# Kernel optimization log

Measured on AMD Instinct MI355X. Metric: run time of the kernel, lower is better.

The kernel has to match this reference:

```python
import jax, jax.numpy as jnp
import numpy as np

LOG2 = float(np.log(2.0))
INV_SQRT3 = float(1.0 / np.sqrt(3.0))

def ssp(x):
    # ShiftedSoftPlus: softplus(x) - log(2)
    return jax.nn.softplus(x) - LOG2

def setup_inputs() -> dict:
    key = jax.random.key(0)
    ks = jax.random.split(key, 13)
    N, E, M, A, R, H = 50000, 800000, 32, 16, 8, 64
    return {
        "node_feats": jax.random.normal(ks[0], (N, 4 * M), dtype=jnp.float32),  # 32x0e + 32x1o flat
        "node_attrs": jax.random.normal(ks[1], (N, A), dtype=jnp.float32),
        "edge_embedding": jax.random.uniform(ks[2], (E, R), dtype=jnp.float32),  # radial basis, 0e
        "edge_attrs": jax.random.normal(ks[3], (E, 4), dtype=jnp.float32),  # SH: 1x0e + 1x1o
        "edge_index": jax.random.randint(ks[4], (2, E), 0, N),
        "W1s": jax.random.normal(ks[5], (M, M), dtype=jnp.float32),
        "W1v": jax.random.normal(ks[6], (M, M), dtype=jnp.float32),
        "Wr0": jax.random.normal(ks[7], (R, H), dtype=jnp.float32),
        "Wr1": jax.random.normal(ks[8], (H, 4 * M), dtype=jnp.float32),  # tp.weight_numel = 4 paths * 32 mul
        "W2s": jax.random.normal(ks[9], (2 * M, M), dtype=jnp.float32),
        "W2v": jax.random.normal(ks[10], (2 * M, M), dtype=jnp.float32),
        "Wsc_s": jax.random.normal(ks[11], (M, A, M), dtype=jnp.float32),
        "Wsc_v": jax.random.normal(ks[12], (M, A, M), dtype=jnp.float32),
    }

def reference(node_feats, node_attrs, edge_embedding, edge_attrs, edge_index,
              W1s, W1v, Wr0, Wr1, W2s, W2v, Wsc_s, Wsc_v):
    N = node_feats.shape[0]
    M = 32           # multiplicity of each irrep
    A = node_attrs.shape[1]
    AVG_NEIGH = 16.0
    # split flat irreps features: [N,32] scalars (0e), [N,32,3] vectors (1o)
    s_in = node_feats[:, :M]
    v_in = node_feats[:, M:].reshape(N, M, 3)

    # linear_1: per-irrep channel mixing, e3nn 1/sqrt(fan_in) normalization
    inv_m = 1.0 / float(np.sqrt(M))
    s = (s_in @ W1s) * inv_m                                  # [N,32]
    v = jnp.einsum('nmc,mk->nkc', v_in, W1v) * inv_m          # [N,32,3]

    # radial MLP on edge scalars -> per-edge tensor-product path weights [E,4,32]
    h = ssp((edge_embedding @ Wr0) * (1.0 / float(np.sqrt(edge_embedding.shape[1]))))
    w = (h @ Wr1) * (1.0 / float(np.sqrt(h.shape[1])))
    w = w.reshape(-1, 4, M)
    w0, w1, w2, w3 = w[:, 0], w[:, 1], w[:, 2], w[:, 3]

    src, dst = edge_index[0], edge_index[1]
    ss = s[src]                                               # [E,32]
    vv = v[src]                                               # [E,32,3]
    e0 = edge_attrs[:, :1]                                    # [E,1]  Y_0
    e1 = edge_attrs[:, 1:4]                                   # [E,3]  Y_1

    # weighted CG tensor product, 'uvu' paths (component normalization)
    m0 = w0 * ss * e0                                                   # 0e x 0e -> 0e
    m3 = w3 * jnp.einsum('emc,ec->em', vv, e1) * INV_SQRT3              # 1o x 1o -> 0e
    m1 = w1[:, :, None] * ss[:, :, None] * e1[:, None, :]               # 0e x 1o -> 1o
    m2 = w2[:, :, None] * vv * e0[:, :, None]                           # 1o x 0e -> 1o
    mid_s = jnp.concatenate([m0, m3], axis=1)                           # [E,64]
    mid_v = jnp.concatenate([m1, m2], axis=1)                           # [E,64,3]

    # scatter-sum to destination nodes
    ns = jax.ops.segment_sum(mid_s, dst, num_segments=N)
    nv = jax.ops.segment_sum(mid_v, dst, num_segments=N)
    neigh = 1.0 / float(np.sqrt(AVG_NEIGH))

    # linear_2 on simplified mid irreps 64x0e + 64x1o
    inv2 = 1.0 / float(np.sqrt(2 * M))
    out_s = (ns @ W2s) * (inv2 * neigh)
    out_v = jnp.einsum('nmc,mk->nkc', nv, W2v) * (inv2 * neigh)

    # self connection: FullyConnectedTensorProduct(node_feats_in, node_attrs)
    fc = 1.0 / float(np.sqrt(M * A))
    out_s = out_s + jnp.einsum('nu,na,uaw->nw', s_in, node_attrs, Wsc_s) * fc
    out_v = out_v + jnp.einsum('nuc,na,uaw->nwc', v_in, node_attrs, Wsc_v) * fc

    return jnp.concatenate([out_s, out_v.reshape(N, 3 * M)], axis=1)
```

## Files before the change

### kernel.cpp

```cpp
#include <hip/hip_runtime.h>
#include <stdint.h>
#include <math.h>

typedef __attribute__((ext_vector_type(8))) short bf16x8;
typedef __attribute__((ext_vector_type(4))) float f32x4;

__device__ __forceinline__ unsigned short f2bf(float f){
  unsigned int u = __float_as_uint(f);
  u += 0x7fffu + ((u >> 16) & 1u);
  return (unsigned short)(u >> 16);
}

__device__ __forceinline__ float bf2f(short s){
  return __uint_as_float(((unsigned int)(unsigned short)s) << 16);
}

__device__ __forceinline__ float ssp_f(float x){
  float u = exp2f(-fabsf(x)*1.4426950408889634f);
  return fmaxf(x, 0.f) + 0.6931471805599453f*(__log2f(1.0f + u) - 1.0f);
}

__global__ void k_count_prep(const int* __restrict__ eidx, int E, int* __restrict__ cnt,
                             const float* __restrict__ Wr0, const float* __restrict__ Wr1,
                             const float* __restrict__ Wsc_s, const float* __restrict__ Wsc_v,
                             const float* __restrict__ W1s, const float* __restrict__ W1v,
                             unsigned short* __restrict__ wr1frag, float* __restrict__ wr0p,
                             unsigned short* __restrict__ wscfrag, unsigned short* __restrict__ w1frag){
  int id = blockIdx.x*256 + threadIdx.x;
  if(id < 512) wr0p[id] = Wr0[(id & 7)*64 + (id >> 3)];
  if(id < 1024){
    int fi = id >> 6, lane = id & 63;
    int c0 = lane & 15, g = lane >> 4;
    int kt = fi >> 3, ct = fi & 7;
    unsigned short tmp[8];
    #pragma unroll
    for(int i = 0; i < 8; i++){
      int k = kt*32 + g*8 + i;
      tmp[i] = f2bf(Wr1[k*128 + ct*16 + c0]);
    }
    #pragma unroll
    for(int i = 0; i < 8; i++) wr1frag[id*8 + i] = tmp[i];
  }
  if(id < 4096){
    int sel  = id >> 11;
    int fi   = (id >> 6) & 31;
    int lane = id & 63;
    int c0 = lane & 15, g = lane >> 4;
    int ks = fi >> 1, ct = fi & 1;
    const float* W = sel ? Wsc_v : Wsc_s;
    bf16x8 tmp;
    #pragma unroll
    for(int i = 0; i < 8; i++){
      int k = ks*32 + g*8 + i;
      tmp[i] = (short)f2bf(W[k*32 + ct*16 + c0]);
    }
    *(bf16x8*)&wscfrag[(size_t)id*8] = tmp;
  }
  if(id < 256){
    int sel = id >> 7, ct = (id >> 6) & 1, lane = id & 63;
    int c0 = lane & 15, g = lane >> 4;
    const float* W = sel ? W1v : W1s;
    bf16x8 tmp;
    #pragma unroll
    for(int i = 0; i < 8; i++){
      int m = g*8 + i;
      tmp[i] = (short)f2bf(W[m*32 + ct*16 + c0]);
    }
    *(bf16x8*)&w1frag[(size_t)id*8] = tmp;
  }
  if(id < E) atomicAdd(&cnt[eidx[E + id]], 1);
}

__global__ void k_scan_a(const int* __restrict__ cnt, int N, int* __restrict__ offs, int* __restrict__ bsum){
  __shared__ int arr[1024];
  int t = threadIdx.x, i = blockIdx.x*1024 + t;
  int v = (i < N) ? cnt[i] : 0;
  int own = v;
  arr[t] = v;
  for(int off = 1; off < 1024; off <<= 1){
    __syncthreads();
    int u = (t >= off) ? arr[t - off] : 0;
    __syncthreads();
    arr[t] += u;
  }
  if(i < N) offs[i] = arr[t] - own;
  if(t == 1023) bsum[blockIdx.x] = arr[1023];
}

__global__ void k_scan_b(int* __restrict__ bsum, int NB, int* __restrict__ offs, int N){
  if(threadIdx.x == 0 && blockIdx.x == 0){
    int run = 0;
    for(int b = 0; b < NB; b++){ int t = bsum[b]; bsum[b] = run; run += t; }
    offs[N] = run;
  }
}

__global__ void k_scan_c(int* __restrict__ offs, const int* __restrict__ bsum, int* __restrict__ cursor, int N){
  int i = blockIdx.x*1024 + threadIdx.x;
  if(i < N){
    int v = offs[i] + bsum[blockIdx.x];
    offs[i] = v;
    cursor[i] = v;
  }
}

__global__ void k_perm(const float* __restrict__ eemb, const float* __restrict__ eattr,
                       const int* __restrict__ eidx, int E, int* __restrict__ cursor,
                       int* __restrict__ src_perm, float* __restrict__ eattr_perm,
                       float* __restrict__ eemb_perm){
  int e = blockIdx.x*256 + threadIdx.x;
  if(e < E){
    int d = eidx[E + e];
    int dp = atomicAdd(&cursor[d], 1);
    src_perm[dp] = eidx[e];
    *(f32x4*)(eattr_perm + (size_t)dp*4) = *(const f32x4*)(eattr + (size_t)e*4);
    *(f32x4*)(eemb_perm + (size_t)dp*8)     = *(const f32x4*)(eemb + (size_t)e*8);
    *(f32x4*)(eemb_perm + (size_t)dp*8 + 4) = *(const f32x4*)(eemb + (size_t)e*8 + 4);
  }
}

__global__ __launch_bounds__(256) void k_node(
    const float* __restrict__ nf, const float* __restrict__ na,
    const unsigned short* __restrict__ w1frag,
    const unsigned short* __restrict__ wscfrag,
    unsigned short* __restrict__ sv, float* __restrict__ out, int N)
{
  __shared__ float xl[64*133];
  __shared__ __align__(16) float al[64*20];
  const int t = threadIdx.x;
  const int n0 = blockIdx.x*64;

  for(int idx = t; idx < 64*128; idx += 256){
    int r = idx >> 7, c = idx & 127;
    int n = n0 + r;
    xl[r*133 + c] = (n < N) ? nf[(size_t)n*128 + c] : 0.f;
  }
  for(int idx = t; idx < 64*16; idx += 256){
    int r = idx >> 4, c = idx & 15;
    int n = n0 + r;
    al[r*20 + c] = (n < N) ? na[(size_t)n*16 + c] : 0.f;
  }
  __syncthreads();

  const float INVM = 0.17677669529663689f;
  const float FC   = 0.044194173824159216f;

  const int lane = t & 63, wv = t >> 6;
  const int c0 = lane & 15, g = lane >> 4;

  {
    const unsigned short* w1f = w1frag + (size_t)((wv == 0) ? 0 : 1024);
    bf16x8 b0 = *(const bf16x8*)&w1f[(0*64 + lane)*8];
    bf16x8 b1 = *(const bf16x8*)&w1f[(1*64 + lane)*8];
    #pragma unroll
    for(int rt = 0; rt < 4; rt++){
      int row = rt*16 + c0;
      bf16x8 a;
      #pragma unroll
      for(int i = 0; i < 8; i++){
        int m = g*8 + i;
        float xv = (wv == 0) ? xl[row*133 + m] : xl[row*133 + 32 + 3*m + (wv-1)];
        a[i] = (short)f2bf(xv);
      }
      f32x4 z = {0.f,0.f,0.f,0.f};
      f32x4 d0 = __builtin_amdgcn_mfma_f32_16x16x32_bf16(a, b0, z, 0, 0, 0);
      f32x4 d1 = __builtin_amdgcn_mfma_f32_16x16x32_bf16(a, b1, z, 0, 0, 0);
      #pragma unroll
      for(int r = 0; r < 4; r++){
        int node = n0 + rt*16 + g*4 + r;
        if(node < N){
          sv[(size_t)node*128 + c0*8 + wv*2 + 0] = f2bf(d0[r]*INVM);
          sv[(size_t)node*128 + c0*8 + wv*2 + 1] = f2bf(d1[r]*INVM);
        }
      }
    }
  }

  const unsigned short* wf = wscfrag + (size_t)((wv == 0) ? 0 : 16384);

  f32x4 accm[4][2];
  #pragma unroll
  for(int rt = 0; rt < 4; rt++)
    #pragma unroll
    for(int ct = 0; ct < 2; ct++) accm[rt][ct] = (f32x4){0.f,0.f,0.f,0.f};

  for(int ks = 0; ks < 16; ks++){
    bf16x8 bfr[2];
    bfr[0] = *(const bf16x8*)&wf[(size_t)((ks*2 + 0)*64 + lane)*8];
    bfr[1] = *(const bf16x8*)&wf[(size_t)((ks*2 + 1)*64 + lane)*8];
    int u2 = ks*2 + (g >> 1);
    int ab = (g & 1)*8;
    #pragma unroll
    for(int rt = 0; rt < 4; rt++){
      int row = rt*16 + c0;
      float xv = (wv == 0) ? xl[row*133 + u2] : xl[row*133 + 32 + 3*u2 + (wv-1)];
      f32x4 v0 = *(const f32x4*)&al[row*20 + ab];
      f32x4 v1 = *(const f32x4*)&al[row*20 + ab + 4];
      bf16x8 a;
      a[0] = (short)f2bf(xv*v0[0]); a[1] = (short)f2bf(xv*v0[1]);
      a[2] = (short)f2bf(xv*v0[2]); a[3] = (short)f2bf(xv*v0[3]);
      a[4] = (short)f2bf(xv*v1[0]); a[5] = (short)f2bf(xv*v1[1]);
      a[6] = (short)f2bf(xv*v1[2]); a[7] = (short)f2bf(xv*v1[3]);
      #pragma unroll
      for(int ct = 0; ct < 2; ct++)
        accm[rt][ct] = __builtin_amdgcn_mfma_f32_16x16x32_bf16(a, bfr[ct], accm[rt][ct], 0, 0, 0);
    }
  }

  #pragma unroll
  for(int rt = 0; rt < 4; rt++)
    #pragma unroll
    for(int ct = 0; ct < 2; ct++)
      #pragma unroll
      for(int i = 0; i < 4; i++){
        int node = n0 + rt*16 + g*4 + i;
        if(node < N){
          int col = ct*16 + c0;
          float v = accm[rt][ct][i] * FC;
          if(wv == 0) out[(size_t)node*128 + col] = v;
          else        out[(size_t)node*128 + 32 + 3*col + (wv-1)] = v;
        }
      }
}

__global__ __launch_bounds__(256, 4) void k_wedge(
    const float* __restrict__ eemb_perm,
    const unsigned short* __restrict__ wr1frag, const float* __restrict__ wr0p,
    unsigned short* __restrict__ wper, int NB16, int E)
{
  __shared__ __align__(16) float wr0t[512];
  __shared__ __align__(16) unsigned short bwl[8192];
  const int t = threadIdx.x;
  {
    const f32x4* s4 = (const f32x4*)wr1frag;
    f32x4* d4 = (f32x4*)bwl;
    #pragma unroll
    for(int i = 0; i < 4; i++) d4[t + i*256] = s4[t + i*256];
    if(t < 128) ((f32x4*)wr0t)[t] = ((const f32x4*)wr0p)[t];
  }
  __syncthreads();

  const int lane = t & 63;
  const int wv   = t >> 6;
  const int c0   = lane & 15;
  const int g    = lane >> 4;
  const float S8 = 0.35355339059327373f;

  int p = blockIdx.x*4 + wv;
  if(p >= NB16) return;
  int p16 = p*16;
  int bc = E - p16; if(bc > 16) bc = 16;
  bool val = (c0 < bc);

  size_t row = (size_t)(p16 + (val ? c0 : 0))*8;
  f32x4 p0 = *(const f32x4*)(eemb_perm + row);
  f32x4 p1 = *(const f32x4*)(eemb_perm + row + 4);
  float ee[8];
  ee[0]=p0[0]; ee[1]=p0[1]; ee[2]=p0[2]; ee[3]=p0[3];
  ee[4]=p1[0]; ee[5]=p1[1]; ee[6]=p1[2]; ee[7]=p1[3];

  bf16x8 afr[2];
  #pragma unroll
  for(int kt = 0; kt < 2; kt++){
    bf16x8 a;
    #pragma unroll
    for(int i = 0; i < 8; i++){
      int j = kt*32 + g*8 + i;
      f32x4 wa = *(const f32x4*)&wr0t[j*8];
      f32x4 wb = *(const f32x4*)&wr0t[j*8 + 4];
      float pre = ee[0]*wa[0] + ee[1]*wa[1] + ee[2]*wa[2] + ee[3]*wa[3]
                + ee[4]*wb[0] + ee[5]*wb[1] + ee[6]*wb[2] + ee[7]*wb[3];
      a[i] = (short)f2bf(ssp_f(pre * S8));
    }
    afr[kt] = a;
  }

  f32x4 cfr[8];
  #pragma unroll
  for(int ct = 0; ct < 8; ct++) cfr[ct] = (f32x4){0.f,0.f,0.f,0.f};
  #pragma unroll
  for(int kt = 0; kt < 2; kt++)
    #pragma unroll
    for(int ct = 0; ct < 8; ct++){
      bf16x8 bfr = *(const bf16x8*)&bwl[((kt*8 + ct)*64 + lane)*8];
      cfr[ct] = __builtin_amdgcn_mfma_f32_16x16x32_bf16(afr[kt], bfr, cfr[ct], 0, 0, 0);
    }

  #pragma unroll
  for(int i = 0; i < 4; i++){
    if(g*4 + i < bc){
      bf16x8 wpk;
      #pragma unroll
      for(int ct = 0; ct < 8; ct++) wpk[ct] = (short)f2bf(cfr[ct][i] * 0.125f);
      *(bf16x8*)(wper + (size_t)(p16 + g*4 + i)*128 + c0*8) = wpk;
    }
  }
}

__global__ __launch_bounds__(256, 4) void k_msg(
    const unsigned short* __restrict__ sv, const unsigned short* __restrict__ wper,
    const float* __restrict__ eattr_perm, const int* __restrict__ src_perm,
    const int* __restrict__ offs, const float* __restrict__ W2s,
    const float* __restrict__ W2v, float* __restrict__ out, int N)
{
  __shared__ __align__(16) float nsl[4][256];
  __shared__ __align__(16) float w2sT[32*68];
  __shared__ __align__(16) float w2vT[32*68];
  const int t = threadIdx.x, lane = t & 63, wv = t >> 6;
  const int c0 = lane & 15, g = lane >> 4;

  {
    #pragma unroll
    for(int i = 0; i < 8; i++){
      int idx = t + i*256;
      int m = idx >> 5, o = idx & 31;
      w2sT[o*68 + m] = W2s[idx];
      w2vT[o*68 + m] = W2v[idx];
    }
  }
  __syncthreads();

  const int n = blockIdx.x*4 + wv;
  if(n >= N) return;

  const float SC2 = 0.03125f;
  const float IS3 = 0.57735026918962576f;

  float acc[16];
  #pragma unroll
  for(int i = 0; i < 16; i++) acc[i] = 0.f;

  const int eb0 = offs[n], eb1 = offs[n+1];
  for(int eb = eb0; eb < eb1; eb += 16){
    int bc = eb1 - eb; if(bc > 16) bc = 16;
    #pragma unroll
    for(int r = 0; r < 4; r++){
      int es = r*4 + g;
      if(es >= bc) continue;
      int e = eb + es;
      int s = src_perm[e];
      bf16x8 sr = *(const bf16x8*)(sv + (size_t)s*128 + c0*8);
      f32x4 ea = *(const f32x4*)(eattr_perm + (size_t)e*4);
      bf16x8 w8 = *(const bf16x8*)(wper + (size_t)e*128 + c0*8);
      float w0A = bf2f(w8[0]), w0B = bf2f(w8[1]);
      float w1A = bf2f(w8[2]), w1B = bf2f(w8[3]);
      float w2A = bf2f(w8[4]), w2B = bf2f(w8[5]);
      float w3A = bf2f(w8[6]), w3B = bf2f(w8[7]);
      float ssA = bf2f(sr[0]), ssB = bf2f(sr[1]);
      float vA0 = bf2f(sr[2]), vB0 = bf2f(sr[3]);
      float vA1 = bf2f(sr[4]), vB1 = bf2f(sr[5]);
      float vA2 = bf2f(sr[6]), vB2 = bf2f(sr[7]);
      float e0 = ea[0], e1x = ea[1], e1y = ea[2], e1z = ea[3];

      acc[0] += w0A*ssA*e0;
      acc[1] += w0B*ssB*e0;
      acc[2] += w3A*(vA0*e1x + vA1*e1y + vA2*e1z);
      acc[3] += w3B*(vB0*e1x + vB1*e1y + vB2*e1z);
      float h1A = w1A*ssA, h1B = w1B*ssB;
      acc[4]  += h1A*e1x; acc[5]  += h1A*e1y; acc[6]  += h1A*e1z;
      acc[7]  += h1B*e1x; acc[8]  += h1B*e1y; acc[9]  += h1B*e1z;
      float h2A = w2A*e0, h2B = w2B*e0;
      acc[10] += h2A*vA0; acc[11] += h2A*vA1; acc[12] += h2A*vA2;
      acc[13] += h2B*vB0; acc[14] += h2B*vB1; acc[15] += h2B*vB2;
    }
  }

  #pragma unroll
  for(int i = 0; i < 16; i++){
    acc[i] += __shfl_xor(acc[i], 16);
    acc[i] += __shfl_xor(acc[i], 32);
  }

  float* nl = nsl[wv];
  if(g == 0){
    nl[c0]      = acc[0];
    nl[16 + c0] = acc[1];
    nl[32 + c0] = acc[2]*IS3;
    nl[48 + c0] = acc[3]*IS3;
    #pragma unroll
    for(int cc = 0; cc < 3; cc++){
      nl[64 + cc*64 +  0 + c0] = acc[4  + cc];
      nl[64 + cc*64 + 16 + c0] = acc[7  + cc];
      nl[64 + cc*64 + 32 + c0] = acc[10 + cc];
      nl[64 + cc*64 + 48 + c0] = acc[13 + cc];
    }
  }
  __threadfence_block();

  const int t1 = lane, t2 = 64 + lane;
  int u1 = t1 - 32; if(u1 < 0) u1 = 0;
  const int w1i = u1/3, c1i = u1%3;
  const int w2i = (t2 - 32)/3, c2i = (t2 - 32)%3;
  const f32x4* p1a = (const f32x4*)((t1 < 32) ? &nl[0] : &nl[64 + c1i*64]);
  const f32x4* p1b = (const f32x4*)((t1 < 32) ? &w2sT[t1*68] : &w2vT[w1i*68]);
  const f32x4* p2a = (const f32x4*)&nl[64 + c2i*64];
  const f32x4* p2b = (const f32x4*)&w2vT[w2i*68];
  float s1 = 0.f, s2 = 0.f;
  #pragma unroll
  for(int q = 0; q < 16; q++){
    f32x4 a = p1a[q], b = p1b[q];
    f32x4 c = p2a[q], d = p2b[q];
    s1 += a[0]*b[0] + a[1]*b[1] + a[2]*b[2] + a[3]*b[3];
    s2 += c[0]*d[0] + c[1]*d[1] + c[2]*d[2] + c[3]*d[3];
  }
  out[(size_t)n*128 + t1] += s1*SC2;
  out[(size_t)n*128 + t2] += s2*SC2;
}

extern "C" void kernel_launch(void* const* d_in, const int* in_sizes, int n_in,
                              void* d_out, int out_size, void* d_ws, size_t ws_size,
                              hipStream_t stream)
{
  const float* nf    = (const float*)d_in[0];
  const float* na    = (const float*)d_in[1];
  const float* eemb  = (const float*)d_in[2];
  const float* eattr = (const float*)d_in[3];
  const int*   eidx  = (const int*)d_in[4];
  const float* W1s   = (const float*)d_in[5];
  const float* W1v   = (const float*)d_in[6];
  const float* Wr0   = (const float*)d_in[7];
  const float* Wr1   = (const float*)d_in[8];
  const float* W2s   = (const float*)d_in[9];
  const float* W2v   = (const float*)d_in[10];
  const float* Wsc_s = (const float*)d_in[11];
  const float* Wsc_v = (const float*)d_in[12];
  float* out = (float*)d_out;

  int N = in_sizes[0]/128;
  int E = in_sizes[2]/8;
  int NB16 = (E + 15)/16;

  char* ws = (char*)d_ws;
  size_t off = 0;
  unsigned short* sv = (unsigned short*)(ws + off); off += (size_t)N*128*2;
  unsigned short* wper = (unsigned short*)(ws + off); off += (size_t)NB16*16*128*2;
  float* eemb_perm = (float*)(ws + off);      off += (size_t)NB16*16*8*4;
  float* eattr_perm = (float*)(ws + off);     off += (size_t)NB16*16*4*4;
  int* src_perm = (int*)(ws + off);           off += (size_t)NB16*16*4;
  int* cnt    = (int*)(ws + off);             off += (size_t)N*4;
  int* offs   = (int*)(ws + off);             off += (size_t)(N+1)*4;
  int* cursor = (int*)(ws + off);             off += (size_t)N*4;
  int* bsum   = (int*)(ws + off);             off += 4096;
  unsigned short* wr1frag = (unsigned short*)(ws + off); off += 16384;
  float* wr0p = (float*)(ws + off);           off += 2048;
  unsigned short* wscfrag = (unsigned short*)(ws + off); off += 65536;
  unsigned short* w1frag = (unsigned short*)(ws + off);  off += 4096;

  int NB = (N + 1023)/1024;

  (void)hipMemsetAsync(cnt, 0, (size_t)N*4, stream);
  k_count_prep<<<dim3((E+255)/256), dim3(256), 0, stream>>>(eidx, E, cnt, Wr0, Wr1,
                                                            Wsc_s, Wsc_v, W1s, W1v,
                                                            wr1frag, wr0p, wscfrag, w1frag);
  k_scan_a <<<dim3(NB),          dim3(1024),0, stream>>>(cnt, N, offs, bsum);
  k_scan_b <<<dim3(1),           dim3(64),  0, stream>>>(bsum, NB, offs, N);
  k_scan_c <<<dim3(NB),          dim3(1024),0, stream>>>(offs, bsum, cursor, N);
  k_perm   <<<dim3((E+255)/256), dim3(256), 0, stream>>>(eemb, eattr, eidx, E, cursor,
                                                         src_perm, eattr_perm, eemb_perm);
  k_node   <<<dim3((N+63)/64),   dim3(256), 0, stream>>>(nf, na, w1frag, wscfrag, sv, out, N);
  k_wedge  <<<dim3((NB16+3)/4),  dim3(256), 0, stream>>>(eemb_perm, wr1frag, wr0p, wper, NB16, E);
  k_msg    <<<dim3((N+3)/4),     dim3(256), 0, stream>>>(sv, wper, eattr_perm, src_perm, offs,
                                                         W2s, W2v, out, N);
}
```

Before: 337.9 us.

## Split linear_2 out of message kernel into separate bf16 MFMA kernel

The per-node W2 projection moves out of k_msg, which used scalar FP32 dot products and loaded the transposed W2 into LDS in every block. k_msg now stores the aggregated 256-wide node message as bf16 to a buffer that reuses the eemb_perm workspace. A new k_out kernel applies W2s/W2v with bf16 MFMA over 64-node tiles, using weight fragments pre-packed in the prep kernel. This lightens k_msg (no LDS weight staging, fewer registers) at the cost of an extra launch, a bf16 round trip of node messages through global memory, and reduced precision in the projection.

```diff
diff --git a/kernel.cpp b/kernel.cpp
--- a/kernel.cpp
+++ b/kernel.cpp
@@ -3,6 +3,7 @@
 #include <math.h>
 
 typedef __attribute__((ext_vector_type(8))) short bf16x8;
+typedef __attribute__((ext_vector_type(4))) short s16x4;
 typedef __attribute__((ext_vector_type(4))) float f32x4;
 
 __device__ __forceinline__ unsigned short f2bf(float f){
@@ -24,8 +25,10 @@
                              const float* __restrict__ Wr0, const float* __restrict__ Wr1,
                              const float* __restrict__ Wsc_s, const float* __restrict__ Wsc_v,
                              const float* __restrict__ W1s, const float* __restrict__ W1v,
+                             const float* __restrict__ W2s, const float* __restrict__ W2v,
                              unsigned short* __restrict__ wr1frag, float* __restrict__ wr0p,
-                             unsigned short* __restrict__ wscfrag, unsigned short* __restrict__ w1frag){
+                             unsigned short* __restrict__ wscfrag, unsigned short* __restrict__ w1frag,
+                             unsigned short* __restrict__ w2frag){
   int id = blockIdx.x*256 + threadIdx.x;
   if(id < 512) wr0p[id] = Wr0[(id & 7)*64 + (id >> 3)];
   if(id < 1024){
@@ -67,6 +70,19 @@
       tmp[i] = (short)f2bf(W[m*32 + ct*16 + c0]);
     }
     *(bf16x8*)&w1frag[(size_t)id*8] = tmp;
+  }
+  if(id < 512){
+    int fi = id >> 6, lane = id & 63;
+    int c0 = lane & 15, g = lane >> 4;
+    int sel = fi >> 2, kt = (fi >> 1) & 1, ct = fi & 1;
+    const float* W = sel ? W2v : W2s;
+    bf16x8 tmp;
+    #pragma unroll
+    for(int i = 0; i < 8; i++){
+      int k = kt*32 + g*8 + i;
+      tmp[i] = (short)f2bf(W[k*32 + ct*16 + c0]);
+    }
+    *(bf16x8*)&w2frag[(size_t)id*8] = tmp;
   }
   if(id < E) atomicAdd(&cnt[eidx[E + id]], 1);
 }
@@ -300,30 +316,15 @@
 __global__ __launch_bounds__(256, 4) void k_msg(
     const unsigned short* __restrict__ sv, const unsigned short* __restrict__ wper,
     const float* __restrict__ eattr_perm, const int* __restrict__ src_perm,
-    const int* __restrict__ offs, const float* __restrict__ W2s,
-    const float* __restrict__ W2v, float* __restrict__ out, int N)
+    const int* __restrict__ offs, unsigned short* __restrict__ nsv, int N)
 {
   __shared__ __align__(16) float nsl[4][256];
-  __shared__ __align__(16) float w2sT[32*68];
-  __shared__ __align__(16) float w2vT[32*68];
   const int t = threadIdx.x, lane = t & 63, wv = t >> 6;
   const int c0 = lane & 15, g = lane >> 4;
 
-  {
-    #pragma unroll
-    for(int i = 0; i < 8; i++){
-      int idx = t + i*256;
-      int m = idx >> 5, o = idx & 31;
-      w2sT[o*68 + m] = W2s[idx];
-      w2vT[o*68 + m] = W2v[idx];
-    }
-  }
-  __syncthreads();
-
   const int n = blockIdx.x*4 + wv;
   if(n >= N) return;
 
-  const float SC2 = 0.03125f;
   const float IS3 = 0.57735026918962576f;
 
   float acc[16];
@@ -387,24 +388,56 @@
   }
   __threadfence_block();
 
-  const int t1 = lane, t2 = 64 + lane;
-  int u1 = t1 - 32; if(u1 < 0) u1 = 0;
-  const int w1i = u1/3, c1i = u1%3;
-  const int w2i = (t2 - 32)/3, c2i = (t2 - 32)%3;
-  const f32x4* p1a = (const f32x4*)((t1 < 32) ? &nl[0] : &nl[64 + c1i*64]);
-  const f32x4* p1b = (const f32x4*)((t1 < 32) ? &w2sT[t1*68] : &w2vT[w1i*68]);
-  const f32x4* p2a = (const f32x4*)&nl[64 + c2i*64];
-  const f32x4* p2b = (const f32x4*)&w2vT[w2i*68];
-  float s1 = 0.f, s2 = 0.f;
-  #pragma unroll
-  for(int q = 0; q < 16; q++){
-    f32x4 a = p1a[q], b = p1b[q];
-    f32x4 c = p2a[q], d = p2b[q];
-    s1 += a[0]*b[0] + a[1]*b[1] + a[2]*b[2] + a[3]*b[3];
-    s2 += c[0]*d[0] + c[1]*d[1] + c[2]*d[2] + c[3]*d[3];
-  }
-  out[(size_t)n*128 + t1] += s1*SC2;
-  out[(size_t)n*128 + t2] += s2*SC2;
+  f32x4 v4 = *(const f32x4*)&nl[lane*4];
+  s16x4 o4;
+  o4[0] = (short)f2bf(v4[0]); o4[1] = (short)f2bf(v4[1]);
+  o4[2] = (short)f2bf(v4[2]); o4[3] = (short)f2bf(v4[3]);
+  *(s16x4*)(nsv + (size_t)n*256 + lane*4) = o4;
+}
+
+__global__ __launch_bounds__(256) void k_out(
+    const unsigned short* __restrict__ nsv, const unsigned short* __restrict__ w2frag,
+    float* __restrict__ out, int N)
+{
+  const int t = threadIdx.x, lane = t & 63, wv = t >> 6;
+  const int c0 = lane & 15, g = lane >> 4;
+  const int n0 = blockIdx.x*64;
+  const float SC2 = 0.03125f;
+  const int sel = (wv == 0) ? 0 : 1;
+
+  bf16x8 bfr[2][2];
+  #pragma unroll
+  for(int kt = 0; kt < 2; kt++)
+    #pragma unroll
+    for(int ct = 0; ct < 2; ct++)
+      bfr[kt][ct] = *(const bf16x8*)&w2frag[(size_t)(((sel*2 + kt)*2 + ct)*64 + lane)*8];
+
+  #pragma unroll
+  for(int rt = 0; rt < 4; rt++){
+    int na_ = n0 + rt*16 + c0; if(na_ >= N) na_ = N - 1;
+    const unsigned short* ap = nsv + (size_t)na_*256 + wv*64;
+    bf16x8 a0 = *(const bf16x8*)(ap + g*8);
+    bf16x8 a1 = *(const bf16x8*)(ap + 32 + g*8);
+    f32x4 accq[2];
+    #pragma unroll
+    for(int ct = 0; ct < 2; ct++){
+      f32x4 z = {0.f,0.f,0.f,0.f};
+      f32x4 d = __builtin_amdgcn_mfma_f32_16x16x32_bf16(a0, bfr[0][ct], z, 0, 0, 0);
+      d = __builtin_amdgcn_mfma_f32_16x16x32_bf16(a1, bfr[1][ct], d, 0, 0, 0);
+      accq[ct] = d;
+    }
+    #pragma unroll
+    for(int ct = 0; ct < 2; ct++)
+      #pragma unroll
+      for(int i = 0; i < 4; i++){
+        int node = n0 + rt*16 + g*4 + i;
+        if(node < N){
+          int col = ct*16 + c0;
+          size_t idx = (size_t)node*128 + ((wv == 0) ? col : 32 + 3*col + (wv-1));
+          out[idx] += accq[ct][i]*SC2;
+        }
+      }
+  }
 }
 
 extern "C" void kernel_launch(void* const* d_in, const int* in_sizes, int n_in,
@@ -435,6 +468,7 @@
   unsigned short* sv = (unsigned short*)(ws + off); off += (size_t)N*128*2;
   unsigned short* wper = (unsigned short*)(ws + off); off += (size_t)NB16*16*128*2;
   float* eemb_perm = (float*)(ws + off);      off += (size_t)NB16*16*8*4;
+  unsigned short* nsv = (unsigned short*)eemb_perm;
   float* eattr_perm = (float*)(ws + off);     off += (size_t)NB16*16*4*4;
   int* src_perm = (int*)(ws + off);           off += (size_t)NB16*16*4;
   int* cnt    = (int*)(ws + off);             off += (size_t)N*4;
@@ -445,13 +479,14 @@
   float* wr0p = (float*)(ws + off);           off += 2048;
   unsigned short* wscfrag = (unsigned short*)(ws + off); off += 65536;
   unsigned short* w1frag = (unsigned short*)(ws + off);  off += 4096;
+  unsigned short* w2frag = (unsigned short*)(ws + off);  off += 8192;
 
   int NB = (N + 1023)/1024;
 
   (void)hipMemsetAsync(cnt, 0, (size_t)N*4, stream);
   k_count_prep<<<dim3((E+255)/256), dim3(256), 0, stream>>>(eidx, E, cnt, Wr0, Wr1,
-                                                            Wsc_s, Wsc_v, W1s, W1v,
-                                                            wr1frag, wr0p, wscfrag, w1frag);
+                                                            Wsc_s, Wsc_v, W1s, W1v, W2s, W2v,
+                                                            wr1frag, wr0p, wscfrag, w1frag, w2frag);
   k_scan_a <<<dim3(NB),          dim3(1024),0, stream>>>(cnt, N, offs, bsum);
   k_scan_b <<<dim3(1),           dim3(64),  0, stream>>>(bsum, NB, offs, N);
   k_scan_c <<<dim3(NB),          dim3(1024),0, stream>>>(offs, bsum, cursor, N);
@@ -460,5 +495,6 @@
   k_node   <<<dim3((N+63)/64),   dim3(256), 0, stream>>>(nf, na, w1frag, wscfrag, sv, out, N);
   k_wedge  <<<dim3((NB16+3)/4),  dim3(256), 0, stream>>>(eemb_perm, wr1frag, wr0p, wper, NB16, E);
   k_msg    <<<dim3((N+3)/4),     dim3(256), 0, stream>>>(sv, wper, eattr_perm, src_perm, offs,
-                                                         W2s, W2v, out, N);
-}
+                                                         nsv, N);
+  k_out    <<<dim3((N+63)/64),   dim3(256), 0, stream>>>(nsv, w2frag, out, N);
+}
```

After: 343.3 us. No clear change (+1.6%).
